# Performance work log

Hardware: AMD Instinct MI355X
Metric: run time of the kernel (lower is better)

## Reference

```python
import jax, jax.numpy as jnp
import numpy as np
from functools import partial

N = 100000
E = 1600000
F_IN, F_HID, F_OUT = 128, 128, 64


def setup_inputs() -> dict:
    key = jax.random.key(0)
    ks = jax.random.split(key, 10)
    x = jax.random.normal(ks[0], (N, F_IN), dtype=jnp.float32)
    edge_index = jax.random.randint(ks[1], (2, E), 0, N, dtype=jnp.int64)
    edge_attr = jax.random.uniform(ks[2], (E,), dtype=jnp.float32)
    # GCNConv params: Linear(in, out, bias=False) weight + separate bias
    def glorot(k, fan_in, fan_out):
        lim = jnp.sqrt(6.0 / (fan_in + fan_out))
        return jax.random.uniform(k, (fan_in, fan_out), minval=-lim, maxval=lim, dtype=jnp.float32)
    return {
        "x": x, "edge_index": edge_index, "edge_attr": edge_attr,
        "W1": glorot(ks[3], F_IN, F_HID),  "b1": jnp.zeros((F_HID,), jnp.float32),
        "W2": glorot(ks[4], F_HID, F_HID), "b2": jnp.zeros((F_HID,), jnp.float32),
        "W3": glorot(ks[5], F_HID, F_OUT), "b3": jnp.zeros((F_OUT,), jnp.float32),
    }


def _gcn_norm(src, dst, ew, n):
    # PyG gcn_norm: add self-loops with weight 1, symmetric normalization.
    loop = jnp.arange(n, dtype=src.dtype)
    src_f = jnp.concatenate([src, loop])
    dst_f = jnp.concatenate([dst, loop])
    ew_f = jnp.concatenate([ew, jnp.ones((n,), ew.dtype)])
    deg = jax.ops.segment_sum(ew_f, dst_f, num_segments=n)
    dinv = jnp.where(deg > 0, jax.lax.rsqrt(deg), 0.0)
    norm = dinv[src_f] * ew_f * dinv[dst_f]  # [E+N]
    return src_f, dst_f, norm


def _gcn_conv(x, W, b, src_f, dst_f, norm, n):
    h = x @ W  # [N, out]
    msg = norm[:, None] * h[src_f]  # gather + per-edge scale
    out = jax.ops.segment_sum(msg, dst_f, num_segments=n)  # scatter-add
    return out + b


def reference(x, edge_index, edge_attr, W1, b1, W2, b2, W3, b3):
    n = x.shape[0]
    src, dst = edge_index[0], edge_index[1]
    src_f, dst_f, norm = _gcn_norm(src, dst, edge_attr, n)
    h = jax.nn.relu(_gcn_conv(x, W1, b1, src_f, dst_f, norm, n))
    h = jax.nn.relu(_gcn_conv(h, W2, b2, src_f, dst_f, norm, n))
    out = _gcn_conv(h, W3, b3, src_f, dst_f, norm, n)
    return jax.nn.log_softmax(out, axis=-1)
```

## Files before the change

kernel.cpp:

```cpp
#include <hip/hip_runtime.h>

typedef unsigned short ushortT;
typedef unsigned int uintT;
typedef unsigned long long ullT;
typedef __attribute__((ext_vector_type(8))) short bf16x8;
typedef __attribute__((ext_vector_type(4))) float f32x4;

#define NBUCK 391
#define EPB   4096
#define NBEB  391
#define BSLOT 4608

union H16 { ushortT u; _Float16 h; };

__device__ __forceinline__ float bf2f(uintT u16) {
    return __uint_as_float(u16 << 16);
}
__device__ __forceinline__ float bflo(uintT u) {
    return __uint_as_float(u << 16);
}
__device__ __forceinline__ float bfhi(uintT u) {
    return __uint_as_float(u & 0xffff0000u);
}
__device__ __forceinline__ ushortT f2bf(float f) {
    unsigned int u = __float_as_uint(f);
    unsigned int r = (u + 0x7fffu + ((u >> 16) & 1u)) >> 16;
    return (ushortT)r;
}

#define ACC8(U, W) \
    acc[0] = fmaf(W, bflo(U.x), acc[0]); acc[1] = fmaf(W, bfhi(U.x), acc[1]); \
    acc[2] = fmaf(W, bflo(U.y), acc[2]); acc[3] = fmaf(W, bfhi(U.y), acc[3]); \
    acc[4] = fmaf(W, bflo(U.z), acc[4]); acc[5] = fmaf(W, bfhi(U.z), acc[5]); \
    acc[6] = fmaf(W, bflo(U.w), acc[6]); acc[7] = fmaf(W, bfhi(U.w), acc[7]);


__device__ __forceinline__ void twist_body(const float* W, ushortT* Wt, int K, int C, int idx) {
    if (idx < K * C) {
        int k = idx / C, c = idx - k * C;
        Wt[c * K + k] = f2bf(W[idx]);
    }
}

template <int C, bool ABF16>
__device__ __forceinline__ void gemm_body(const void* Aop, const ushortT* Wt,
                                          ushortT* outp, int nrows, int bid, int tid) {
    const int K = 128;
    int wv = tid >> 6;
    int ln = tid & 63;
    int row0 = (bid * 4 + wv) * 16;
    if (row0 >= nrows) return;
    int rA = ln & 15;
    int kg = ln >> 4;
    int rowA = row0 + rA;
    bool okA = rowA < nrows;

    bf16x8 af[4];
    if (ABF16) {
        const ushortT* A = (const ushortT*)Aop;
        #pragma unroll
        for (int kb = 0; kb < 4; ++kb) {
            if (okA) af[kb] = *(const bf16x8*)(A + (size_t)rowA * K + kb * 32 + kg * 8);
            else     af[kb] = (bf16x8)(short)0;
        }
    } else {
        const float* A = (const float*)Aop;
        #pragma unroll
        for (int kb = 0; kb < 4; ++kb) {
            bf16x8 t = (bf16x8)(short)0;
            if (okA) {
                const float4* ap = reinterpret_cast<const float4*>(A + (size_t)rowA * K + kb * 32 + kg * 8);
                float4 p0 = ap[0], p1 = ap[1];
                t[0] = (short)f2bf(p0.x); t[1] = (short)f2bf(p0.y);
                t[2] = (short)f2bf(p0.z); t[3] = (short)f2bf(p0.w);
                t[4] = (short)f2bf(p1.x); t[5] = (short)f2bf(p1.y);
                t[6] = (short)f2bf(p1.z); t[7] = (short)f2bf(p1.w);
            }
            af[kb] = t;
        }
    }

    int colB = ln & 15;
    f32x4 acc[C / 16];
    #pragma unroll
    for (int nt = 0; nt < C / 16; ++nt) acc[nt] = (f32x4)0.0f;
    #pragma unroll
    for (int nt = 0; nt < C / 16; ++nt) {
        int c = nt * 16 + colB;
        #pragma unroll
        for (int kb = 0; kb < 4; ++kb) {
            bf16x8 bfr = *(const bf16x8*)(Wt + c * K + kb * 32 + kg * 8);
            acc[nt] = __builtin_amdgcn_mfma_f32_16x16x32_bf16(af[kb], bfr, acc[nt], 0, 0, 0);
        }
    }
    #pragma unroll
    for (int nt = 0; nt < C / 16; ++nt) {
        #pragma unroll
        for (int r = 0; r < 4; ++r) {
            int rowC = row0 + (ln >> 4) * 4 + r;
            if (rowC < nrows) outp[(size_t)rowC * C + nt * 16 + colB] = f2bf(acc[nt][r]);
        }
    }
}

__global__ __launch_bounds__(512) void k_sort_twist(const int* src, const int* dst, const float* ew,
                                                    int* bucket_count, ullT* erec, int e,
                                                    const float* W1, ushortT* Wt1,
                                                    const float* W2, ushortT* Wt2,
                                                    const float* W3, ushortT* Wt3) {
    __shared__ ullT srec[EPB];
    __shared__ int  gaddr[EPB];
    __shared__ int  hist[512];
    __shared__ int  adj[NBUCK];
    int blk = blockIdx.x, t = threadIdx.x;
    if (blk >= NBEB) {
        int tb = blk - NBEB;
        if (tb < 32)      twist_body(W1, Wt1, 128, 128, tb * 512 + t);
        else if (tb < 64) twist_body(W2, Wt2, 128, 128, (tb - 32) * 512 + t);
        else              twist_body(W3, Wt3, 128, 64, (tb - 64) * 512 + t);
        return;
    }
    hist[t] = 0;
    __syncthreads();
    int base = blk * EPB;
    for (int j = t; j < EPB; j += 512) {
        int i = base + j;
        if (i < e) atomicAdd(&hist[dst[i] >> 8], 1);
    }
    __syncthreads();
    int myc = hist[t];
    for (int off = 1; off < 512; off <<= 1) {
        int x = 0; if (t >= off) x = hist[t - off];
        __syncthreads();
        if (t >= off) hist[t] += x;
        __syncthreads();
    }
    int lb = (t == 0) ? 0 : hist[t - 1];
    __syncthreads();
    hist[t] = lb;
    if (t < NBUCK) {
        int gb = 0;
        if (myc > 0) gb = atomicAdd(&bucket_count[t], myc);
        adj[t] = t * BSLOT + gb - lb;
    }
    __syncthreads();
    for (int j = t; j < EPB; j += 512) {
        int i = base + j;
        if (i < e) {
            int d = dst[i];
            int b = d >> 8;
            int pos = atomicAdd(&hist[b], 1);
            H16 cv; cv.h = (_Float16)ew[i];
            ullT rec = ((ullT)(uintT)src[i] << 24) | ((ullT)(uintT)(d & 255) << 16) | (ullT)cv.u;
            srec[pos] = rec;
            int ga = adj[b] + pos;
            int lim = b * BSLOT + BSLOT - 1;
            gaddr[pos] = ga <= lim ? ga : lim;
        }
    }
    __syncthreads();
    int m = e - base; if (m > EPB) m = EPB;
    for (int k = t; k < m; k += 512) {
        erec[(size_t)gaddr[k]] = srec[k];
    }
}

__global__ __launch_bounds__(256) void k_bucket_gemm1(const ullT* erec,
                                                      const int* bucket_count,
                                                      uintT* entries, float* dinv, int* counts, int n,
                                                      const float* x, const ushortT* Wt1,
                                                      ushortT* hw1) {
    __shared__ int cnt[256];
    __shared__ uintT wsum[256];
    int blk = blockIdx.x, t = threadIdx.x;
    if (blk < NBUCK) {
        int b = blk;
        cnt[t] = 0; wsum[t] = 0;
        __syncthreads();
        int beg = b * BSLOT, m = bucket_count[b];
        if (m > BSLOT) m = BSLOT;
        for (int j = t; j < m; j += 256) {
            ullT rec = erec[(size_t)beg + j];
            int dlow = (int)((rec >> 16) & 255);
            ushortT hu = (ushortT)(rec & 0xffffu);
            int slot = atomicAdd(&cnt[dlow], 1);
            H16 cv; cv.u = hu;
            atomicAdd(&wsum[dlow], (uintT)__float2uint_rn((float)cv.h * 16777216.0f));
            if (slot < 64) {
                uintT s = (uintT)(rec >> 24);
                entries[((size_t)b * 256 + dlow) * 64 + slot] = (s << 15) | (uintT)hu;
            }
        }
        __syncthreads();
        int node = b * 256 + t;
        if (node < n) {
            float sum = (float)wsum[t] * (1.0f / 16777216.0f);
            dinv[node] = rsqrtf(1.0f + sum);
            int c = cnt[t];
            counts[node] = c > 64 ? 64 : c;
        }
    } else {
        gemm_body<128, false>(x, Wt1, hw1, n, blk - NBUCK, t);
    }
}

template <int C>
__global__ __launch_bounds__(256) void k_agg_gemm(const char* hwb, const float* dinv,
                                                  const int* counts, const uintT* entries,
                                                  const float* bias, const ushortT* Wt,
                                                  ushortT* outp, int n) {
    __shared__ ullT wp[4][64];
    __shared__ uintT rows[16][64];
    int wv = threadIdx.x >> 6, ln = threadIdx.x & 63;
    int tile0 = blockIdx.x * 16;
    int lg = ln & 15;
    int gp = ln >> 4;

    float wfac4[4], wsrc4[4];
    int   cnt4[4];
    uintT ent4[4];
    #pragma unroll
    for (int nn = 0; nn < 4; ++nn) {
        int i = tile0 + wv * 4 + nn;
        wfac4[nn] = dinv[i];
        cnt4[nn]  = counts[i];
        ent4[nn]  = entries[(size_t)i * 64 + ln];
        wsrc4[nn] = dinv[(int)(ent4[nn] >> 15)];
    }

    const char* lane_base = hwb + (size_t)(lg * 16);

    #pragma unroll
    for (int nn = 0; nn < 4; ++nn) {
        int r = wv * 4 + nn;
        int i = tile0 + r;
        float wfac = wfac4[nn];
        int cnt = cnt4[nn];
        int cntp = (cnt + 7) & ~7;
        uintT ent = ent4[nn];
        int s_l = (ln < cnt) ? (int)(ent >> 15) : 0;
        H16 cv; cv.u = (ushortT)(ent & 0x7fffu);
        float w_l = (ln < cnt) ? wsrc4[nn] * (float)cv.h * wfac : 0.f;
        uintT soff = (ln < cnt) ? ((uintT)s_l << 8) : 0u;
        wp[wv][ln] = ((ullT)__float_as_uint(w_l) << 32) | (ullT)soff;
        const ullT* wpw = wp[wv];

        uint4 uself = *(const uint4*)(lane_base + (size_t)i * 256);

        float acc[8];
        #pragma unroll
        for (int j = 0; j < 8; ++j) acc[j] = 0.f;

        ullT pa = wpw[gp], pb = wpw[4 + gp];
        uint4 ua = *(const uint4*)(lane_base + (uintT)pa);
        uint4 ub = *(const uint4*)(lane_base + (uintT)pb);
        for (int e = 8; e < cntp; e += 8) {
            ullT pa2 = wpw[e + gp], pb2 = wpw[e + 4 + gp];
            uint4 ua2 = *(const uint4*)(lane_base + (uintT)pa2);
            uint4 ub2 = *(const uint4*)(lane_base + (uintT)pb2);
            float wa = __uint_as_float((uintT)(pa >> 32));
            float wb = __uint_as_float((uintT)(pb >> 32));
            ACC8(ua, wa)
            ACC8(ub, wb)
            pa = pa2; pb = pb2; ua = ua2; ub = ub2;
        }
        {
            float wa = __uint_as_float((uintT)(pa >> 32));
            float wb = __uint_as_float((uintT)(pb >> 32));
            ACC8(ua, wa)
            ACC8(ub, wb)
        }

        #pragma unroll
        for (int j = 0; j < 8; ++j) {
            acc[j] += __shfl_xor(acc[j], 16);
            acc[j] += __shfl_xor(acc[j], 32);
        }
        float selfw = wfac * wfac;
        ACC8(uself, selfw)

        float a0 = (gp & 1) ? ((gp & 2) ? acc[6] : acc[2]) : ((gp & 2) ? acc[4] : acc[0]);
        float a1 = (gp & 1) ? ((gp & 2) ? acc[7] : acc[3]) : ((gp & 2) ? acc[5] : acc[1]);
        int d = lg * 4 + gp;
        float2 bs = *(const float2*)(bias + 2 * d);
        a0 = fmaxf(a0 + bs.x, 0.f);
        a1 = fmaxf(a1 + bs.y, 0.f);
        uintT packed = (uintT)f2bf(a0) | ((uintT)f2bf(a1) << 16);
        rows[r][((d * 4) ^ ((r & 7) << 4)) >> 2] = packed;
    }
    __syncthreads();

    {
        int rA = ln & 15;
        int kg = ln >> 4;
        int colB = ln & 15;
        const char* rbase = (const char*)&rows[0][0];
        bf16x8 af[4];
        #pragma unroll
        for (int kb = 0; kb < 4; ++kb) {
            int byteoff = (kb * 64 + kg * 16) ^ ((rA & 7) << 4);
            af[kb] = *(const bf16x8*)(rbase + rA * 256 + byteoff);
        }
        const int NS = C / 64;
        #pragma unroll
        for (int s = 0; s < NS; ++s) {
            int nt = wv * NS + s;
            f32x4 gac = (f32x4)0.0f;
            int c = nt * 16 + colB;
            #pragma unroll
            for (int kb = 0; kb < 4; ++kb) {
                bf16x8 bfr = *(const bf16x8*)(Wt + c * 128 + kb * 32 + kg * 8);
                gac = __builtin_amdgcn_mfma_f32_16x16x32_bf16(af[kb], bfr, gac, 0, 0, 0);
            }
            #pragma unroll
            for (int r = 0; r < 4; ++r) {
                int rowC = tile0 + kg * 4 + r;
                outp[(size_t)rowC * C + nt * 16 + colB] = f2bf(gac[r]);
            }
        }
    }
}

__global__ __launch_bounds__(256) void k_agg_softmax(const char* hwb, const float* dinv,
                                                     const int* counts, const uintT* entries,
                                                     const float* bias, float* outp, int n) {
    __shared__ ullT wp[4][64];
    int wv = threadIdx.x >> 6, ln = threadIdx.x & 63;
    int i = blockIdx.x * 4 + wv;
    if (i >= n) return;
    int lg = ln & 7;
    int gp = ln >> 3;

    float wfac = dinv[i];
    int cnt = counts[i];
    int cntp = (cnt + 7) & ~7;
    uintT ent = entries[(size_t)i * 64 + ln];
    int s_l = (ln < cnt) ? (int)(ent >> 15) : 0;
    H16 cv; cv.u = (ushortT)(ent & 0x7fffu);
    float w_l = (ln < cnt) ? dinv[s_l] * (float)cv.h * wfac : 0.f;
    wp[wv][ln] = ((ullT)__float_as_uint(w_l) << 32) | (ullT)((uintT)s_l << 7);
    const ullT* wpw = wp[wv];

    const char* lane_base = hwb + (size_t)(lg * 16);
    uint4 uself = *(const uint4*)(lane_base + (size_t)i * 128);

    float acc[8];
    #pragma unroll
    for (int j = 0; j < 8; ++j) acc[j] = 0.f;

    ullT pa = wpw[gp];
    uint4 ua = *(const uint4*)(lane_base + (uintT)pa);
    for (int e = 8; e < cntp; e += 8) {
        ullT pa2 = wpw[e + gp];
        uint4 ua2 = *(const uint4*)(lane_base + (uintT)pa2);
        float wa = __uint_as_float((uintT)(pa >> 32));
        ACC8(ua, wa)
        pa = pa2; ua = ua2;
    }
    {
        float wa = __uint_as_float((uintT)(pa >> 32));
        ACC8(ua, wa)
    }

    #pragma unroll
    for (int j = 0; j < 8; ++j) {
        acc[j] += __shfl_xor(acc[j], 8);
        acc[j] += __shfl_xor(acc[j], 16);
        acc[j] += __shfl_xor(acc[j], 32);
    }
    float selfw = wfac * wfac;
    ACC8(uself, selfw)

    float4 bsa = *(const float4*)(bias + lg * 8);
    float4 bsb = *(const float4*)(bias + lg * 8 + 4);
    acc[0] += bsa.x; acc[1] += bsa.y; acc[2] += bsa.z; acc[3] += bsa.w;
    acc[4] += bsb.x; acc[5] += bsb.y; acc[6] += bsb.z; acc[7] += bsb.w;

    float m = acc[0];
    #pragma unroll
    for (int j = 1; j < 8; ++j) m = fmaxf(m, acc[j]);
    m = fmaxf(m, __shfl_xor(m, 1));
    m = fmaxf(m, __shfl_xor(m, 2));
    m = fmaxf(m, __shfl_xor(m, 4));
    float s = 0.f;
    #pragma unroll
    for (int j = 0; j < 8; ++j) s += __expf(acc[j] - m);
    s += __shfl_xor(s, 1);
    s += __shfl_xor(s, 2);
    s += __shfl_xor(s, 4);
    float ls = m + __logf(s);

    float v0 = (gp & 1) ? acc[4] : acc[0];
    float v1 = (gp & 1) ? acc[5] : acc[1];
    float v2 = (gp & 1) ? acc[6] : acc[2];
    float v3 = (gp & 1) ? acc[7] : acc[3];
    if (gp < 2) {
        float4 r = { v0 - ls, v1 - ls, v2 - ls, v3 - ls };
        *(float4*)(outp + (size_t)i * 64 + lg * 8 + gp * 4) = r;
    }
}

extern "C" void kernel_launch(void* const* d_in, const int* in_sizes, int n_in,
                              void* d_out, int out_size, void* d_ws, size_t ws_size,
                              hipStream_t stream) {
    const int N = 100000, E = 1600000;
    const int NPAD = NBUCK * 256;
    const float* x  = (const float*)d_in[0];
    const int*   src = (const int*)d_in[1];
    const int*   dst = src + E;
    const float* ea = (const float*)d_in[2];
    const float* W1 = (const float*)d_in[3];
    const float* b1 = (const float*)d_in[4];
    const float* W2 = (const float*)d_in[5];
    const float* b2 = (const float*)d_in[6];
    const float* W3 = (const float*)d_in[7];
    const float* b3 = (const float*)d_in[8];
    float* outp = (float*)d_out;

    char* ws = (char*)d_ws;
    auto alloc = [&](size_t bytes) {
        char* p = ws;
        ws += (bytes + 255) & ~(size_t)255;
        return p;
    };
    int*   bucket_count = (int*)alloc((size_t)NBUCK * 4);
    ullT*  erec         = (ullT*)alloc((size_t)NBUCK * BSLOT * 8);
    float* dinv    = (float*)alloc((size_t)N * 4);
    int*   counts  = (int*)  alloc((size_t)N * 4);
    uintT* entries = (uintT*)alloc((size_t)NPAD * 64 * 4);
    ushortT* Wt1   = (ushortT*)alloc(128 * 128 * 2);
    ushortT* Wt2   = (ushortT*)alloc(128 * 128 * 2);
    ushortT* Wt3   = (ushortT*)alloc(128 * 64 * 2);
    ushortT* hwA   = (ushortT*)alloc((size_t)N * 128 * 2);
    ushortT* hwB   = (ushortT*)alloc((size_t)N * 128 * 2);

    const int nbGemm = (N + 63) / 64;
    const int nbFused = N / 16;
    const int nbAgg  = (N + 3) / 4;

    hipMemsetAsync(bucket_count, 0, (size_t)NBUCK * 4, stream);
    k_sort_twist<<<NBEB + 80, 512, 0, stream>>>(src, dst, ea, bucket_count, erec, E,
                                                W1, Wt1, W2, Wt2, W3, Wt3);
    k_bucket_gemm1<<<NBUCK + nbGemm, 256, 0, stream>>>(erec, bucket_count,
                                                       entries, dinv, counts, N,
                                                       x, Wt1, hwA);
    k_agg_gemm<128><<<nbFused, 256, 0, stream>>>((const char*)hwA, dinv, counts, entries,
                                                 b1, Wt2, hwB, N);
    k_agg_gemm<64><<<nbFused, 256, 0, stream>>>((const char*)hwB, dinv, counts, entries,
                                                b2, Wt3, hwA, N);
    k_agg_softmax<<<nbAgg, 256, 0, stream>>>((const char*)hwA, dinv, counts, entries,
                                             b3, outp, N);
}
```

Baseline: 363.8 us.

## Balance row aggregation across waves dynamically and deepen gather prefetch in final layer

In the aggregate+GEMM kernel, the per-row weight tables for all 16 rows are built into shared memory up front, and waves then claim rows through a shared atomic counter instead of each owning four fixed rows. This targets load imbalance from uneven in-degrees. The final-layer aggregation also moves from a 2-stage to a 3-stage software pipeline on the gathered feature loads to hide more memory latency. The cost is more shared memory, an extra barrier and atomics, and more live registers.

```diff
diff --git a/kernel.cpp b/kernel.cpp
--- a/kernel.cpp
+++ b/kernel.cpp
@@ -209,41 +209,47 @@
                                                   const int* counts, const uintT* entries,
                                                   const float* bias, const ushortT* Wt,
                                                   ushortT* outp, int n) {
-    __shared__ ullT wp[4][64];
+    __shared__ ullT wp[16][64];
     __shared__ uintT rows[16][64];
+    __shared__ float wfac16[16];
+    __shared__ int   cnt16[16];
+    __shared__ int   cur;
     int wv = threadIdx.x >> 6, ln = threadIdx.x & 63;
     int tile0 = blockIdx.x * 16;
     int lg = ln & 15;
     int gp = ln >> 4;
 
-    float wfac4[4], wsrc4[4];
-    int   cnt4[4];
-    uintT ent4[4];
-    #pragma unroll
-    for (int nn = 0; nn < 4; ++nn) {
-        int i = tile0 + wv * 4 + nn;
-        wfac4[nn] = dinv[i];
-        cnt4[nn]  = counts[i];
-        ent4[nn]  = entries[(size_t)i * 64 + ln];
-        wsrc4[nn] = dinv[(int)(ent4[nn] >> 15)];
-    }
-
-    const char* lane_base = hwb + (size_t)(lg * 16);
+    if (threadIdx.x == 0) cur = 0;
 
     #pragma unroll
     for (int nn = 0; nn < 4; ++nn) {
         int r = wv * 4 + nn;
         int i = tile0 + r;
-        float wfac = wfac4[nn];
-        int cnt = cnt4[nn];
+        float wfac = dinv[i];
+        int cnt = counts[i];
+        uintT ent = entries[(size_t)i * 64 + ln];
+        float wsrc = dinv[(int)(ent >> 15)];
+        H16 cv; cv.u = (ushortT)(ent & 0x7fffu);
+        float w_l = (ln < cnt) ? wsrc * (float)cv.h * wfac : 0.f;
+        uintT soff = (ln < cnt) ? ((ent >> 15) << 8) : 0u;
+        wp[r][ln] = ((ullT)__float_as_uint(w_l) << 32) | (ullT)soff;
+        if (ln == 0) { wfac16[r] = wfac; cnt16[r] = cnt; }
+    }
+    __syncthreads();
+
+    const char* lane_base = hwb + (size_t)(lg * 16);
+    float2 bs = *(const float2*)(bias + 2 * (lg * 4 + gp));
+
+    for (;;) {
+        int r = 0;
+        if (ln == 0) r = atomicAdd(&cur, 1);
+        r = __shfl(r, 0);
+        if (r >= 16) break;
+        int i = tile0 + r;
+        float wfac = wfac16[r];
+        int cnt = cnt16[r];
         int cntp = (cnt + 7) & ~7;
-        uintT ent = ent4[nn];
-        int s_l = (ln < cnt) ? (int)(ent >> 15) : 0;
-        H16 cv; cv.u = (ushortT)(ent & 0x7fffu);
-        float w_l = (ln < cnt) ? wsrc4[nn] * (float)cv.h * wfac : 0.f;
-        uintT soff = (ln < cnt) ? ((uintT)s_l << 8) : 0u;
-        wp[wv][ln] = ((ullT)__float_as_uint(w_l) << 32) | (ullT)soff;
-        const ullT* wpw = wp[wv];
+        const ullT* wpw = wp[r];
 
         uint4 uself = *(const uint4*)(lane_base + (size_t)i * 256);
 
@@ -281,12 +287,10 @@
 
         float a0 = (gp & 1) ? ((gp & 2) ? acc[6] : acc[2]) : ((gp & 2) ? acc[4] : acc[0]);
         float a1 = (gp & 1) ? ((gp & 2) ? acc[7] : acc[3]) : ((gp & 2) ? acc[5] : acc[1]);
-        int d = lg * 4 + gp;
-        float2 bs = *(const float2*)(bias + 2 * d);
         a0 = fmaxf(a0 + bs.x, 0.f);
         a1 = fmaxf(a1 + bs.y, 0.f);
         uintT packed = (uintT)f2bf(a0) | ((uintT)f2bf(a1) << 16);
-        rows[r][((d * 4) ^ ((r & 7) << 4)) >> 2] = packed;
+        rows[r][(((lg * 4 + gp) * 4) ^ ((r & 7) << 4)) >> 2] = packed;
     }
     __syncthreads();
 
@@ -348,18 +352,30 @@
     #pragma unroll
     for (int j = 0; j < 8; ++j) acc[j] = 0.f;
 
-    ullT pa = wpw[gp];
-    uint4 ua = *(const uint4*)(lane_base + (uintT)pa);
-    for (int e = 8; e < cntp; e += 8) {
-        ullT pa2 = wpw[e + gp];
-        uint4 ua2 = *(const uint4*)(lane_base + (uintT)pa2);
-        float wa = __uint_as_float((uintT)(pa >> 32));
-        ACC8(ua, wa)
-        pa = pa2; ua = ua2;
+    ullT paA = wpw[gp];
+    uint4 uaA = *(const uint4*)(lane_base + (uintT)paA);
+    bool hasB = cntp > 8;
+    ullT paB = 0;
+    uint4 uaB = {0, 0, 0, 0};
+    if (hasB) {
+        paB = wpw[8 + gp];
+        uaB = *(const uint4*)(lane_base + (uintT)paB);
+    }
+    for (int e = 16; e < cntp; e += 8) {
+        ullT paC = wpw[e + gp];
+        uint4 uaC = *(const uint4*)(lane_base + (uintT)paC);
+        float wa = __uint_as_float((uintT)(paA >> 32));
+        ACC8(uaA, wa)
+        paA = paB; uaA = uaB;
+        paB = paC; uaB = uaC;
     }
     {
-        float wa = __uint_as_float((uintT)(pa >> 32));
-        ACC8(ua, wa)
+        float wa = __uint_as_float((uintT)(paA >> 32));
+        ACC8(uaA, wa)
+    }
+    if (hasB) {
+        float wa = __uint_as_float((uintT)(paB >> 32));
+        ACC8(uaB, wa)
     }
 
     #pragma unroll
```

Result: slower. 379.6 us (+4.3%).

## Pre-convert x to bf16 in sort kernel and deepen softmax gather prefetch

Applied to the files above, without the earlier changes.

Moves the fp32-to-bf16 conversion of x out of the layer-1 GEMM into extra blocks of the edge-sort kernel, which write a bf16 copy into the hwB buffer. The first GEMM then reads half as many bytes and does no conversion, and the conversion work overlaps with the sort blocks. Separately, the softmax aggregation loop now keeps two gathered rows in flight instead of one to hide more gather latency. The cost is an extra full write and read of x in bf16 plus many more blocks in the sort launch.

```diff
diff --git a/kernel.cpp b/kernel.cpp
--- a/kernel.cpp
+++ b/kernel.cpp
@@ -10,6 +10,7 @@
 #define EPB   4096
 #define NBEB  391
 #define BSLOT 4608
+#define NCONV 3125
 
 union H16 { ushortT u; _Float16 h; };
 
@@ -42,8 +43,19 @@
     }
 }
 
-template <int C, bool ABF16>
-__device__ __forceinline__ void gemm_body(const void* Aop, const ushortT* Wt,
+__device__ __forceinline__ void conv_body(const float* x, ushortT* xb, int idx) {
+    const float4* xp = reinterpret_cast<const float4*>(x) + (size_t)idx * 2;
+    float4 a = xp[0], b = xp[1];
+    uint4 o;
+    o.x = (uintT)f2bf(a.x) | ((uintT)f2bf(a.y) << 16);
+    o.y = (uintT)f2bf(a.z) | ((uintT)f2bf(a.w) << 16);
+    o.z = (uintT)f2bf(b.x) | ((uintT)f2bf(b.y) << 16);
+    o.w = (uintT)f2bf(b.z) | ((uintT)f2bf(b.w) << 16);
+    *reinterpret_cast<uint4*>(xb + (size_t)idx * 8) = o;
+}
+
+template <int C>
+__device__ __forceinline__ void gemm_body(const ushortT* A, const ushortT* Wt,
                                           ushortT* outp, int nrows, int bid, int tid) {
     const int K = 128;
     int wv = tid >> 6;
@@ -56,28 +68,10 @@
     bool okA = rowA < nrows;
 
     bf16x8 af[4];
-    if (ABF16) {
-        const ushortT* A = (const ushortT*)Aop;
-        #pragma unroll
-        for (int kb = 0; kb < 4; ++kb) {
-            if (okA) af[kb] = *(const bf16x8*)(A + (size_t)rowA * K + kb * 32 + kg * 8);
-            else     af[kb] = (bf16x8)(short)0;
-        }
-    } else {
-        const float* A = (const float*)Aop;
-        #pragma unroll
-        for (int kb = 0; kb < 4; ++kb) {
-            bf16x8 t = (bf16x8)(short)0;
-            if (okA) {
-                const float4* ap = reinterpret_cast<const float4*>(A + (size_t)rowA * K + kb * 32 + kg * 8);
-                float4 p0 = ap[0], p1 = ap[1];
-                t[0] = (short)f2bf(p0.x); t[1] = (short)f2bf(p0.y);
-                t[2] = (short)f2bf(p0.z); t[3] = (short)f2bf(p0.w);
-                t[4] = (short)f2bf(p1.x); t[5] = (short)f2bf(p1.y);
-                t[6] = (short)f2bf(p1.z); t[7] = (short)f2bf(p1.w);
-            }
-            af[kb] = t;
-        }
+    #pragma unroll
+    for (int kb = 0; kb < 4; ++kb) {
+        if (okA) af[kb] = *(const bf16x8*)(A + (size_t)rowA * K + kb * 32 + kg * 8);
+        else     af[kb] = (bf16x8)(short)0;
     }
 
     int colB = ln & 15;
@@ -107,7 +101,8 @@
                                                     int* bucket_count, ullT* erec, int e,
                                                     const float* W1, ushortT* Wt1,
                                                     const float* W2, ushortT* Wt2,
-                                                    const float* W3, ushortT* Wt3) {
+                                                    const float* W3, ushortT* Wt3,
+                                                    const float* x, ushortT* xb) {
     __shared__ ullT srec[EPB];
     __shared__ int  gaddr[EPB];
     __shared__ int  hist[512];
@@ -117,7 +112,8 @@
         int tb = blk - NBEB;
         if (tb < 32)      twist_body(W1, Wt1, 128, 128, tb * 512 + t);
         else if (tb < 64) twist_body(W2, Wt2, 128, 128, (tb - 32) * 512 + t);
-        else              twist_body(W3, Wt3, 128, 64, (tb - 64) * 512 + t);
+        else if (tb < 80) twist_body(W3, Wt3, 128, 64, (tb - 64) * 512 + t);
+        else              conv_body(x, xb, (tb - 80) * 512 + t);
         return;
     }
     hist[t] = 0;
@@ -130,9 +126,9 @@
     __syncthreads();
     int myc = hist[t];
     for (int off = 1; off < 512; off <<= 1) {
-        int x = 0; if (t >= off) x = hist[t - off];
+        int x2 = 0; if (t >= off) x2 = hist[t - off];
         __syncthreads();
-        if (t >= off) hist[t] += x;
+        if (t >= off) hist[t] += x2;
         __syncthreads();
     }
     int lb = (t == 0) ? 0 : hist[t - 1];
@@ -168,7 +164,7 @@
 __global__ __launch_bounds__(256) void k_bucket_gemm1(const ullT* erec,
                                                       const int* bucket_count,
                                                       uintT* entries, float* dinv, int* counts, int n,
-                                                      const float* x, const ushortT* Wt1,
+                                                      const ushortT* xb, const ushortT* Wt1,
                                                       ushortT* hw1) {
     __shared__ int cnt[256];
     __shared__ uintT wsum[256];
@@ -200,7 +196,7 @@
             counts[node] = c > 64 ? 64 : c;
         }
     } else {
-        gemm_body<128, false>(x, Wt1, hw1, n, blk - NBUCK, t);
+        gemm_body<128>(xb, Wt1, hw1, n, blk - NBUCK, t);
     }
 }
 
@@ -238,10 +234,9 @@
         int cnt = cnt4[nn];
         int cntp = (cnt + 7) & ~7;
         uintT ent = ent4[nn];
-        int s_l = (ln < cnt) ? (int)(ent >> 15) : 0;
         H16 cv; cv.u = (ushortT)(ent & 0x7fffu);
         float w_l = (ln < cnt) ? wsrc4[nn] * (float)cv.h * wfac : 0.f;
-        uintT soff = (ln < cnt) ? ((uintT)s_l << 8) : 0u;
+        uintT soff = (ln < cnt) ? ((ent >> 15) << 8) : 0u;
         wp[wv][ln] = ((ullT)__float_as_uint(w_l) << 32) | (ullT)soff;
         const ullT* wpw = wp[wv];
 
@@ -348,18 +343,30 @@
     #pragma unroll
     for (int j = 0; j < 8; ++j) acc[j] = 0.f;
 
-    ullT pa = wpw[gp];
-    uint4 ua = *(const uint4*)(lane_base + (uintT)pa);
-    for (int e = 8; e < cntp; e += 8) {
-        ullT pa2 = wpw[e + gp];
-        uint4 ua2 = *(const uint4*)(lane_base + (uintT)pa2);
-        float wa = __uint_as_float((uintT)(pa >> 32));
-        ACC8(ua, wa)
-        pa = pa2; ua = ua2;
+    ullT paA = wpw[gp];
+    uint4 uaA = *(const uint4*)(lane_base + (uintT)paA);
+    bool hasB = cntp > 8;
+    ullT paB = 0;
+    uint4 uaB = {0, 0, 0, 0};
+    if (hasB) {
+        paB = wpw[8 + gp];
+        uaB = *(const uint4*)(lane_base + (uintT)paB);
+    }
+    for (int e = 16; e < cntp; e += 8) {
+        ullT paC = wpw[e + gp];
+        uint4 uaC = *(const uint4*)(lane_base + (uintT)paC);
+        float wa = __uint_as_float((uintT)(paA >> 32));
+        ACC8(uaA, wa)
+        paA = paB; uaA = uaB;
+        paB = paC; uaB = uaC;
     }
     {
-        float wa = __uint_as_float((uintT)(pa >> 32));
-        ACC8(ua, wa)
+        float wa = __uint_as_float((uintT)(paA >> 32));
+        ACC8(uaA, wa)
+    }
+    if (hasB) {
+        float wa = __uint_as_float((uintT)(paB >> 32));
+        ACC8(uaB, wa)
     }
 
     #pragma unroll
@@ -433,17 +440,18 @@
     ushortT* Wt3   = (ushortT*)alloc(128 * 64 * 2);
     ushortT* hwA   = (ushortT*)alloc((size_t)N * 128 * 2);
     ushortT* hwB   = (ushortT*)alloc((size_t)N * 128 * 2);
+    ushortT* xb    = hwB;
 
     const int nbGemm = (N + 63) / 64;
     const int nbFused = N / 16;
     const int nbAgg  = (N + 3) / 4;
 
     hipMemsetAsync(bucket_count, 0, (size_t)NBUCK * 4, stream);
-    k_sort_twist<<<NBEB + 80, 512, 0, stream>>>(src, dst, ea, bucket_count, erec, E,
-                                                W1, Wt1, W2, Wt2, W3, Wt3);
+    k_sort_twist<<<NBEB + 80 + NCONV, 512, 0, stream>>>(src, dst, ea, bucket_count, erec, E,
+                                                        W1, Wt1, W2, Wt2, W3, Wt3, x, xb);
     k_bucket_gemm1<<<NBUCK + nbGemm, 256, 0, stream>>>(erec, bucket_count,
                                                        entries, dinv, counts, N,
-                                                       x, Wt1, hwA);
+                                                       xb, Wt1, hwA);
     k_agg_gemm<128><<<nbFused, 256, 0, stream>>>((const char*)hwA, dinv, counts, entries,
                                                  b1, Wt2, hwB, N);
     k_agg_gemm<64><<<nbFused, 256, 0, stream>>>((const char*)hwB, dinv, counts, entries,
```

Result: no change. 358.9 us, median of 2 (-1.3%).
